# Kernel optimization log

Measured on AMD Instinct MI355X. Metric: run time of the kernel, lower is better.

Reference implementation:

```python
import jax, jax.numpy as jnp
import numpy as np

B, T, H = 1, 2048, 1024
NH, HD, NKV = 16, 64, 4
G = NH // NKV                    # kv groups == Mamba2 n_groups
SINK, WIN = 128, 256             # attention sinks, sliding window
STATE, KSIZE = 256, 4            # Mamba2 state size, conv kernel
MINT = H                         # Mamba2 intermediate (expand=1) == NH*HD
CONV_DIM = MINT + 2 * G * STATE  # 3072
D_INPROJ = MINT + CONV_DIM + NH  # 4112
INTER = 4096
EPS = 1e-6


def _rmsnorm(x, w):
    v = jnp.mean(jnp.square(x), axis=-1, keepdims=True)
    return x * jax.lax.rsqrt(v + EPS) * w


def _rot_half(t):
    return jnp.concatenate([-t[..., HD // 2:], t[..., :HD // 2]], axis=-1)


def _mamba2(h, in_proj_w, conv_w, conv_b, dt_bias, A_log, Dp, mnorm_w, mout_w):
    # h: [B, L, H] evicted hidden states
    Bm, Lm, _ = h.shape
    proj = h @ in_proj_w                                   # [B,L,D_INPROJ]
    z, xBC, dt = jnp.split(proj, [MINT, MINT + CONV_DIM], axis=-1)
    # causal depthwise conv1d (kernel KSIZE), then SiLU
    xp = jnp.pad(xBC, ((0, 0), (KSIZE - 1, 0), (0, 0)))
    conv = sum(xp[:, k:k + Lm, :] * conv_w[:, k] for k in range(KSIZE)) + conv_b
    xBC = jax.nn.silu(conv)
    xs, Bc, Cc = jnp.split(xBC, [MINT, MINT + G * STATE], axis=-1)
    xs = xs.reshape(Bm, Lm, NH, HD)
    Bc = jnp.repeat(Bc.reshape(Bm, Lm, G, STATE), NH // G, axis=2)  # group->head
    Cc = jnp.repeat(Cc.reshape(Bm, Lm, G, STATE), NH // G, axis=2)
    dt = jax.nn.softplus(dt + dt_bias)                     # [B,L,NH]
    A = -jnp.exp(A_log)                                    # [NH]

    def step(hst, inp):
        xt, bt, ct, dtt = inp  # [B,NH,HD],[B,NH,N],[B,NH,N],[B,NH]
        dA = jnp.exp(dtt * A)[..., None, None]
        hst = hst * dA + (dtt[..., None] * xt)[..., None] * bt[:, :, None, :]
        yt = jnp.einsum('bhdn,bhn->bhd', hst, ct)
        return hst, yt

    h0 = jnp.zeros((Bm, NH, HD, STATE), h.dtype)
    tm = lambda a: jnp.moveaxis(a, 1, 0)
    _, ys = jax.lax.scan(step, h0, (tm(xs), tm(Bc), tm(Cc), tm(dt)))
    y = jnp.moveaxis(ys, 0, 1) + Dp[None, None, :, None] * xs
    y = y.reshape(Bm, Lm, MINT) * jax.nn.silu(z)           # gated
    y = _rmsnorm(y, mnorm_w)
    return y @ mout_w


def _forward(hidden_states, cos, sin, ln1_w, q_w, q_b, k_w, k_b, v_w, v_b, o_w,
             in_proj_w, conv_w, conv_b, dt_bias, A_log, D, mnorm_w, mout_w,
             ln2_w, gate_w, up_w, down_w):
    x = hidden_states
    hn = _rmsnorm(x, ln1_w)
    evict_end = T - WIN
    evicted = hn[:, SINK:evict_end]                       # [B, overflow, H]
    mem_out = _mamba2(evicted, in_proj_w, conv_w, conv_b, dt_bias, A_log, D,
                      mnorm_w, mout_w)                    # [B, overflow, H]
    mem_act = mem_out[:, -1:, :]                          # compressed-memory token
    hc = jnp.concatenate([hn[:, :SINK], mem_act, hn[:, evict_end:]], axis=1)
    cosc = jnp.concatenate([cos[:, :SINK + 1], cos[:, evict_end:]], axis=1)
    sinc = jnp.concatenate([sin[:, :SINK + 1], sin[:, evict_end:]], axis=1)
    Tc = SINK + 1 + WIN                                   # 385 compacted tokens
    q = (hc @ q_w + q_b).reshape(B, Tc, NH, HD)
    k = (hc @ k_w + k_b).reshape(B, Tc, NKV, HD)
    v = (hc @ v_w + v_b).reshape(B, Tc, NKV, HD)
    q = q * cosc[:, :, None, :] + _rot_half(q) * sinc[:, :, None, :]
    k = k * cosc[:, :, None, :] + _rot_half(k) * sinc[:, :, None, :]
    k = jnp.repeat(k, G, axis=2)                          # GQA expand
    v = jnp.repeat(v, G, axis=2)
    scores = jnp.einsum('bqhd,bkhd->bhqk', q, k) * (HD ** -0.5)
    idx = jnp.arange(Tc)
    causal = idx[:, None] >= idx[None, :]
    scores = jnp.where(causal, scores, jnp.finfo(scores.dtype).min)
    attn = jax.nn.softmax(scores, axis=-1)
    ao = jnp.einsum('bhqk,bkhd->bqhd', attn, v).reshape(B, Tc, H)
    # replace mem token output with the full Mamba2 outputs for evicted tokens
    ao = jnp.concatenate([ao[:, :SINK], mem_out, ao[:, SINK + 1:]], axis=1)
    ao = ao @ o_w                                         # [B, T, H]
    h1 = x + ao
    mlp_in = _rmsnorm(h1, ln2_w)
    mlp = (jax.nn.silu(mlp_in @ gate_w) * (mlp_in @ up_w)) @ down_w
    return h1 + mlp


def setup_inputs() -> dict:
    key = jax.random.key(0)
    ks = list(jax.random.split(key, 16))
    def nrm(i, shape, s=0.02):
        return jax.random.normal(ks[i], shape, jnp.float32) * s
    x = jax.random.normal(ks[0], (B, T, H), jnp.float32)
    pos = jnp.arange(T, dtype=jnp.float32)
    inv = 1.0 / (10000.0 ** (jnp.arange(0, HD, 2, dtype=jnp.float32) / HD))
    ang = pos[:, None] * inv[None, :]
    emb = jnp.concatenate([ang, ang], axis=-1)
    cos = jnp.broadcast_to(jnp.cos(emb)[None], (B, T, HD))
    sin = jnp.broadcast_to(jnp.sin(emb)[None], (B, T, HD))
    return {
        'hidden_states': x, 'cos': cos, 'sin': sin,
        'ln1_w': jnp.ones((H,), jnp.float32),
        'q_w': nrm(1, (H, NH * HD)), 'q_b': jnp.zeros((NH * HD,), jnp.float32),
        'k_w': nrm(2, (H, NKV * HD)), 'k_b': jnp.zeros((NKV * HD,), jnp.float32),
        'v_w': nrm(3, (H, NKV * HD)), 'v_b': jnp.zeros((NKV * HD,), jnp.float32),
        'o_w': nrm(4, (NH * HD, H)),
        'in_proj_w': nrm(5, (H, D_INPROJ)),
        'conv_w': nrm(6, (CONV_DIM, KSIZE), 0.2),
        'conv_b': jnp.zeros((CONV_DIM,), jnp.float32),
        'dt_bias': nrm(7, (NH,), 0.5),
        'A_log': jnp.log(jnp.arange(1, NH + 1, dtype=jnp.float32)),
        'D': jnp.ones((NH,), jnp.float32),
        'mnorm_w': jnp.ones((MINT,), jnp.float32),
        'mout_w': nrm(8, (MINT, H)),
        'ln2_w': jnp.ones((H,), jnp.float32),
        'gate_w': nrm(9, (H, INTER)),
        'up_w': nrm(10, (H, INTER)),
        'down_w': nrm(11, (INTER, H)),
    }


def reference(hidden_states, cos, sin, ln1_w, q_w, q_b, k_w, k_b, v_w, v_b, o_w,
              in_proj_w, conv_w, conv_b, dt_bias, A_log, D, mnorm_w, mout_w,
              ln2_w, gate_w, up_w, down_w):
    return _forward(hidden_states, cos, sin, ln1_w, q_w, q_b, k_w, k_b, v_w,
                    v_b, o_w, in_proj_w, conv_w, conv_b, dt_bias, A_log, D,
                    mnorm_w, mout_w, ln2_w, gate_w, up_w, down_w)
```

## Files before the change

kernel.cpp:

```cpp
#include <hip/hip_runtime.h>
#include <hip/hip_bf16.h>
#include <math.h>

#define TLEN 2048
#define HDIM 1024
#define NHEAD 16
#define HEADD 64
#define NKVH 4
#define SINKN 128
#define WINN 256
#define STATEN 256
#define KCONV 4
#define MINTN 1024
#define CONVD 3072
#define DPROJ 4112
#define INTERN 4096
#define LMN 1664
#define TCN 385
#define EPSF 1e-6f
#define SCHUNK 128
#define NCHUNK 13

__device__ __forceinline__ float siluf(float x){ return x / (1.0f + expf(-x)); }
__device__ __forceinline__ float softplusf_(float x){ return fmaxf(x, 0.0f) + log1pf(expf(-fabsf(x))); }

__device__ __forceinline__ float block_sum256(float v, float* sb){
#pragma unroll
  for (int m = 32; m > 0; m >>= 1) v += __shfl_xor(v, m);
  int wid = threadIdx.x >> 6;
  if ((threadIdx.x & 63) == 0) sb[wid] = v;
  __syncthreads();
  return sb[0] + sb[1] + sb[2] + sb[3];
}

__global__ __launch_bounds__(256) void rmsnorm_k(const float* __restrict__ in, const float* __restrict__ w,
                                                 float* __restrict__ out){
  __shared__ float sb[4];
  size_t r = blockIdx.x;
  float4 x = ((const float4*)(in + r*HDIM))[threadIdx.x];
  float ss = block_sum256(x.x*x.x + x.y*x.y + x.z*x.z + x.w*x.w, sb);
  float sc = 1.0f / sqrtf(ss*(1.0f/HDIM) + EPSF);
  float4 wv = ((const float4*)w)[threadIdx.x];
  ((float4*)(out + r*HDIM))[threadIdx.x] =
      make_float4(x.x*sc*wv.x, x.y*sc*wv.y, x.z*sc*wv.z, x.w*sc*wv.w);
}

__global__ __launch_bounds__(256) void gated_rmsnorm_k(const float* __restrict__ ys, const float* __restrict__ proj,
                                                       const float* __restrict__ w, float* __restrict__ out){
  __shared__ float sb[4];
  size_t r = blockIdx.x;
  float4 y = ((const float4*)(ys + r*MINTN))[threadIdx.x];
  float4 z = ((const float4*)(proj + r*DPROJ))[threadIdx.x];
  y.x *= siluf(z.x); y.y *= siluf(z.y); y.z *= siluf(z.z); y.w *= siluf(z.w);
  float ss = block_sum256(y.x*y.x + y.y*y.y + y.z*y.z + y.w*y.w, sb);
  float sc = 1.0f / sqrtf(ss*(1.0f/MINTN) + EPSF);
  float4 wv = ((const float4*)w)[threadIdx.x];
  ((float4*)(out + r*MINTN))[threadIdx.x] =
      make_float4(y.x*sc*wv.x, y.y*sc*wv.y, y.z*sc*wv.z, y.w*sc*wv.w);
}

template<int EPI>
__global__ __launch_bounds__(256) void gemm_k(const float* __restrict__ A, const float* __restrict__ B,
                                              float* __restrict__ C, const float* __restrict__ bias,
                                              const float* __restrict__ extra, int M, int N, int K){
  __shared__ float As[16][132];
  __shared__ float Bs[16][64];
  int tid = threadIdx.x;
  int tx = tid & 15, ty = tid >> 4;
  int m0 = blockIdx.y * 128, n0 = blockIdx.x * 64;
  int ar = tid >> 2, ak = (tid & 3) * 4;
  int bk = tid >> 4, bn = (tid & 15) * 4;
  float acc[8][4];
#pragma unroll
  for (int i = 0; i < 8; i++)
#pragma unroll
    for (int j = 0; j < 4; j++) acc[i][j] = 0.f;

  for (int k0 = 0; k0 < K; k0 += 16){
    float4 a0 = make_float4(0,0,0,0), a1 = make_float4(0,0,0,0), b0 = make_float4(0,0,0,0);
    if (m0 + ar < M)      a0 = *(const float4*)(A + (size_t)(m0+ar)*K + k0 + ak);
    if (m0 + ar + 64 < M) a1 = *(const float4*)(A + (size_t)(m0+ar+64)*K + k0 + ak);
    if (n0 + bn < N)      b0 = *(const float4*)(B + (size_t)(k0+bk)*N + n0 + bn);
    __syncthreads();
    As[ak+0][ar] = a0.x; As[ak+1][ar] = a0.y; As[ak+2][ar] = a0.z; As[ak+3][ar] = a0.w;
    As[ak+0][ar+64] = a1.x; As[ak+1][ar+64] = a1.y; As[ak+2][ar+64] = a1.z; As[ak+3][ar+64] = a1.w;
    *(float4*)&Bs[bk][bn] = b0;
    __syncthreads();
#pragma unroll
    for (int kk = 0; kk < 16; kk++){
      float a[8], b[4];
      *(float4*)(a)   = *(const float4*)&As[kk][ty*8];
      *(float4*)(a+4) = *(const float4*)&As[kk][ty*8+4];
      *(float4*)(b)   = *(const float4*)&Bs[kk][tx*4];
#pragma unroll
      for (int i = 0; i < 8; i++)
#pragma unroll
        for (int j = 0; j < 4; j++) acc[i][j] = fmaf(a[i], b[j], acc[i][j]);
    }
  }
  int n = n0 + tx*4;
  if (n >= N) return;
#pragma unroll
  for (int i = 0; i < 8; i++){
    int m = m0 + ty*8 + i;
    if (m >= M) break;
    float r0 = acc[i][0], r1 = acc[i][1], r2 = acc[i][2], r3 = acc[i][3];
    if (EPI == 1){ r0 += bias[n]; r1 += bias[n+1]; r2 += bias[n+2]; r3 += bias[n+3]; }
    if (EPI == 2){ const float* e = extra + (size_t)m*N + n; r0 += e[0]; r1 += e[1]; r2 += e[2]; r3 += e[3]; }
    *(float4*)(C + (size_t)m*N + n) = make_float4(r0, r1, r2, r3);
  }
}

template<int EPI>
__global__ __launch_bounds__(256) void gemm64_k(const float* __restrict__ A, const float* __restrict__ B,
                                                float* __restrict__ C, const float* __restrict__ bias,
                                                const float* __restrict__ extra, int M, int N, int K){
  __shared__ float As[16][68];
  __shared__ float Bs[16][64];
  int tid = threadIdx.x;
  int tx = tid & 15, ty = tid >> 4;
  int m0 = blockIdx.y * 64, n0 = blockIdx.x * 64;
  int ar = tid >> 2, ak = (tid & 3) * 4;
  int bk = tid >> 4, bn = (tid & 15) * 4;
  float acc[4][4];
#pragma unroll
  for (int i = 0; i < 4; i++)
#pragma unroll
    for (int j = 0; j < 4; j++) acc[i][j] = 0.f;

  for (int k0 = 0; k0 < K; k0 += 16){
    float4 a0 = make_float4(0,0,0,0);
    if (m0 + ar < M) a0 = *(const float4*)(A + (size_t)(m0+ar)*K + k0 + ak);
    float4 b0 = *(const float4*)(B + (size_t)(k0+bk)*N + n0 + bn);
    __syncthreads();
    As[ak+0][ar] = a0.x; As[ak+1][ar] = a0.y; As[ak+2][ar] = a0.z; As[ak+3][ar] = a0.w;
    *(float4*)&Bs[bk][bn] = b0;
    __syncthreads();
#pragma unroll
    for (int kk = 0; kk < 16; kk++){
      float a[4], b[4];
      *(float4*)(a) = *(const float4*)&As[kk][ty*4];
      *(float4*)(b) = *(const float4*)&Bs[kk][tx*4];
#pragma unroll
      for (int i = 0; i < 4; i++)
#pragma unroll
        for (int j = 0; j < 4; j++) acc[i][j] = fmaf(a[i], b[j], acc[i][j]);
    }
  }
  int n = n0 + tx*4;
#pragma unroll
  for (int i = 0; i < 4; i++){
    int m = m0 + ty*4 + i;
    if (m >= M) break;
    float r0 = acc[i][0], r1 = acc[i][1], r2 = acc[i][2], r3 = acc[i][3];
    if (EPI == 1){ r0 += bias[n]; r1 += bias[n+1]; r2 += bias[n+2]; r3 += bias[n+3]; }
    if (EPI == 2){ const float* e = extra + (size_t)m*N + n; r0 += e[0]; r1 += e[1]; r2 += e[2]; r3 += e[3]; }
    *(float4*)(C + (size_t)m*N + n) = make_float4(r0, r1, r2, r3);
  }
}

__global__ __launch_bounds__(256) void gemm_gateup_k(const float* __restrict__ A, const float* __restrict__ G,
                                                     const float* __restrict__ U, float* __restrict__ C,
                                                     int M, int N, int K){
  __shared__ float As[16][132];
  __shared__ float Gs[16][64];
  __shared__ float Us[16][64];
  int tid = threadIdx.x;
  int tx = tid & 15, ty = tid >> 4;
  int m0 = blockIdx.y * 128, n0 = blockIdx.x * 64;
  int ar = tid >> 2, ak = (tid & 3) * 4;
  int bk = tid >> 4, bn = (tid & 15) * 4;
  float accg[8][4], accu[8][4];
#pragma unroll
  for (int i = 0; i < 8; i++)
#pragma unroll
    for (int j = 0; j < 4; j++){ accg[i][j] = 0.f; accu[i][j] = 0.f; }

  for (int k0 = 0; k0 < K; k0 += 16){
    float4 a0 = *(const float4*)(A + (size_t)(m0+ar)*K + k0 + ak);
    float4 a1 = *(const float4*)(A + (size_t)(m0+ar+64)*K + k0 + ak);
    float4 g0 = *(const float4*)(G + (size_t)(k0+bk)*N + n0 + bn);
    float4 u0 = *(const float4*)(U + (size_t)(k0+bk)*N + n0 + bn);
    __syncthreads();
    As[ak+0][ar] = a0.x; As[ak+1][ar] = a0.y; As[ak+2][ar] = a0.z; As[ak+3][ar] = a0.w;
    As[ak+0][ar+64] = a1.x; As[ak+1][ar+64] = a1.y; As[ak+2][ar+64] = a1.z; As[ak+3][ar+64] = a1.w;
    *(float4*)&Gs[bk][bn] = g0;
    *(float4*)&Us[bk][bn] = u0;
    __syncthreads();
#pragma unroll
    for (int kk = 0; kk < 16; kk++){
      float a[8], g[4], u[4];
      *(float4*)(a)   = *(const float4*)&As[kk][ty*8];
      *(float4*)(a+4) = *(const float4*)&As[kk][ty*8+4];
      *(float4*)(g)   = *(const float4*)&Gs[kk][tx*4];
      *(float4*)(u)   = *(const float4*)&Us[kk][tx*4];
#pragma unroll
      for (int i = 0; i < 8; i++)
#pragma unroll
        for (int j = 0; j < 4; j++){
          accg[i][j] = fmaf(a[i], g[j], accg[i][j]);
          accu[i][j] = fmaf(a[i], u[j], accu[i][j]);
        }
    }
  }
  int n = n0 + tx*4;
#pragma unroll
  for (int i = 0; i < 8; i++){
    int m = m0 + ty*8 + i;
    *(float4*)(C + (size_t)m*N + n) =
        make_float4(siluf(accg[i][0])*accu[i][0], siluf(accg[i][1])*accu[i][1],
                    siluf(accg[i][2])*accu[i][2], siluf(accg[i][3])*accu[i][3]);
  }
}

__global__ __launch_bounds__(256) void conv_silu_k(const float* __restrict__ proj, const float* __restrict__ cw,
                                                   const float* __restrict__ cb, float* __restrict__ out){
  int idx = blockIdx.x*256 + threadIdx.x;
  if (idx >= LMN*CONVD) return;
  int c = idx % CONVD;
  int t = idx / CONVD;
  float acc = cb[c];
#pragma unroll
  for (int kk = 0; kk < KCONV; kk++){
    int ts = t + kk - (KCONV-1);
    if (ts >= 0) acc = fmaf(proj[(size_t)ts*DPROJ + MINTN + c], cw[c*KCONV + kk], acc);
  }
  out[idx] = siluf(acc);
}

__global__ __launch_bounds__(256) void dtprep_k(const float* __restrict__ proj, const float* __restrict__ dtb,
                                                const float* __restrict__ alog, float* __restrict__ dt,
                                                float* __restrict__ dA){
  int idx = blockIdx.x*256 + threadIdx.x;
  if (idx >= LMN*NHEAD) return;
  int h = idx & 15, t = idx >> 4;
  float d = softplusf_(proj[(size_t)t*DPROJ + MINTN + CONVD + h] + dtb[h]);
  dt[idx] = d;
  dA[idx] = expf(-d * expf(alog[h]));
}


__global__ __launch_bounds__(64) void chunk_prod_k(const float* __restrict__ dAb, float* __restrict__ aQ){
  int c = blockIdx.x >> 4, h = blockIdx.x & 15;
  int lane = threadIdx.x;
  float p = dAb[(c*SCHUNK + lane)*NHEAD + h] * dAb[(c*SCHUNK + 64 + lane)*NHEAD + h];
#pragma unroll
  for (int m = 32; m > 0; m >>= 1) p *= __shfl_xor(p, m);
  if (lane == 0) aQ[c*NHEAD + h] = p;
}

__global__ __launch_bounds__(256) void scan_local_k(const float* __restrict__ cv, const float* __restrict__ dtb,
                                                    const float* __restrict__ dAb, float* __restrict__ hloc){
  int c = blockIdx.x >> 6;
  int sub = blockIdx.x & 63;
  int h = sub >> 2;
  int d = (sub & 3)*16 + (threadIdx.x >> 4);
  int nc = threadIdx.x & 15;
  int g = h >> 2;
  const float* xp = cv + h*HEADD + d;
  const float* Bp = cv + MINTN + g*STATEN + nc*16;
  int t0 = c*SCHUNK;
  float s[16];
#pragma unroll
  for (int i = 0; i < 16; i++) s[i] = 0.f;

  float4 B0[4], B1[4];
  float x0, dt0, dA0, x1, dt1, dA1;
  {
    size_t o = (size_t)t0*CONVD;
    x0 = xp[o]; dt0 = dtb[t0*NHEAD + h]; dA0 = dAb[t0*NHEAD + h];
    B0[0]=((const float4*)(Bp+o))[0]; B0[1]=((const float4*)(Bp+o))[1];
    B0[2]=((const float4*)(Bp+o))[2]; B0[3]=((const float4*)(Bp+o))[3];
    o = (size_t)(t0+1)*CONVD;
    x1 = xp[o]; dt1 = dtb[(t0+1)*NHEAD + h]; dA1 = dAb[(t0+1)*NHEAD + h];
    B1[0]=((const float4*)(Bp+o))[0]; B1[1]=((const float4*)(Bp+o))[1];
    B1[2]=((const float4*)(Bp+o))[2]; B1[3]=((const float4*)(Bp+o))[3];
  }
  for (int tt = 0; tt < SCHUNK; tt += 2){
    {
      float coef = dt0 * x0;
      const float* bf = (const float*)B0;
#pragma unroll
      for (int i = 0; i < 16; i++) s[i] = fmaf(s[i], dA0, coef*bf[i]);
      int tn = t0 + ((tt+2 < SCHUNK) ? tt+2 : SCHUNK-1);
      size_t o = (size_t)tn*CONVD;
      x0 = xp[o]; dt0 = dtb[tn*NHEAD + h]; dA0 = dAb[tn*NHEAD + h];
      B0[0]=((const float4*)(Bp+o))[0]; B0[1]=((const float4*)(Bp+o))[1];
      B0[2]=((const float4*)(Bp+o))[2]; B0[3]=((const float4*)(Bp+o))[3];
    }
    {
      float coef = dt1 * x1;
      const float* bf = (const float*)B1;
#pragma unroll
      for (int i = 0; i < 16; i++) s[i] = fmaf(s[i], dA1, coef*bf[i]);
      int tn = t0 + ((tt+3 < SCHUNK) ? tt+3 : SCHUNK-1);
      size_t o = (size_t)tn*CONVD;
      x1 = xp[o]; dt1 = dtb[tn*NHEAD + h]; dA1 = dAb[tn*NHEAD + h];
      B1[0]=((const float4*)(Bp+o))[0]; B1[1]=((const float4*)(Bp+o))[1];
      B1[2]=((const float4*)(Bp+o))[2]; B1[3]=((const float4*)(Bp+o))[3];
    }
  }
  size_t base = ((size_t)(c*NHEAD + h)*STATEN + nc*16)*64 + d;
#pragma unroll
  for (int i = 0; i < 16; i++) hloc[base + (size_t)i*64] = s[i];
}

__global__ __launch_bounds__(256) void chunk_combine_k(float* __restrict__ hloc, const float* __restrict__ aQ){
  int e = blockIdx.x*256 + threadIdx.x;
  int h = e >> 14;
  float s = 0.f;
  for (int c = 0; c < NCHUNK; c++){
    float a = aQ[c*NHEAD + h];
    size_t off = (size_t)c*(NHEAD*STATEN*64) + e;
    float tmp = hloc[off];
    hloc[off] = s;
    s = fmaf(s, a, tmp);
  }
}

__global__ __launch_bounds__(256) void scan_out_k(const float* __restrict__ cv, const float* __restrict__ dtb,
                                                  const float* __restrict__ dAb, const float* __restrict__ Dp,
                                                  const float* __restrict__ hstart, float* __restrict__ ys){
  int c = blockIdx.x >> 6;
  int sub = blockIdx.x & 63;
  int h = sub >> 2;
  int d = (sub & 3)*16 + (threadIdx.x >> 4);
  int nc = threadIdx.x & 15;
  int g = h >> 2;
  const float* xp = cv + h*HEADD + d;
  const float* Bp = cv + MINTN + g*STATEN + nc*16;
  const float* Cp = cv + MINTN + 1024 + g*STATEN + nc*16;
  float Dh = Dp[h];
  int t0 = c*SCHUNK;
  float s[16];
  {
    size_t base = ((size_t)(c*NHEAD + h)*STATEN + nc*16)*64 + d;
#pragma unroll
    for (int i = 0; i < 16; i++) s[i] = hstart[base + (size_t)i*64];
  }

  float4 B0[4], C0[4], B1[4], C1[4];
  float x0, dt0, dA0, x1, dt1, dA1;
  {
    size_t o = (size_t)t0*CONVD;
    x0 = xp[o]; dt0 = dtb[t0*NHEAD + h]; dA0 = dAb[t0*NHEAD + h];
    B0[0]=((const float4*)(Bp+o))[0]; B0[1]=((const float4*)(Bp+o))[1];
    B0[2]=((const float4*)(Bp+o))[2]; B0[3]=((const float4*)(Bp+o))[3];
    C0[0]=((const float4*)(Cp+o))[0]; C0[1]=((const float4*)(Cp+o))[1];
    C0[2]=((const float4*)(Cp+o))[2]; C0[3]=((const float4*)(Cp+o))[3];
    o = (size_t)(t0+1)*CONVD;
    x1 = xp[o]; dt1 = dtb[(t0+1)*NHEAD + h]; dA1 = dAb[(t0+1)*NHEAD + h];
    B1[0]=((const float4*)(Bp+o))[0]; B1[1]=((const float4*)(Bp+o))[1];
    B1[2]=((const float4*)(Bp+o))[2]; B1[3]=((const float4*)(Bp+o))[3];
    C1[0]=((const float4*)(Cp+o))[0]; C1[1]=((const float4*)(Cp+o))[1];
    C1[2]=((const float4*)(Cp+o))[2]; C1[3]=((const float4*)(Cp+o))[3];
  }
  for (int tt = 0; tt < SCHUNK; tt += 2){
    {
      int t = t0 + tt;
      float coef = dt0 * x0;
      float accp[4] = {0.f,0.f,0.f,0.f};
      const float* bf = (const float*)B0;
      const float* cf = (const float*)C0;
#pragma unroll
      for (int i = 0; i < 16; i++){
        s[i] = fmaf(s[i], dA0, coef*bf[i]);
        accp[i & 3] = fmaf(s[i], cf[i], accp[i & 3]);
      }
      float accv = (accp[0]+accp[1])+(accp[2]+accp[3]);
      accv += __shfl_xor(accv, 1); accv += __shfl_xor(accv, 2);
      accv += __shfl_xor(accv, 4); accv += __shfl_xor(accv, 8);
      if (nc == 0) ys[(size_t)t*MINTN + h*HEADD + d] = accv + Dh*x0;
      int tn = t0 + ((tt+2 < SCHUNK) ? tt+2 : SCHUNK-1);
      size_t o = (size_t)tn*CONVD;
      x0 = xp[o]; dt0 = dtb[tn*NHEAD + h]; dA0 = dAb[tn*NHEAD + h];
      B0[0]=((const float4*)(Bp+o))[0]; B0[1]=((const float4*)(Bp+o))[1];
      B0[2]=((const float4*)(Bp+o))[2]; B0[3]=((const float4*)(Bp+o))[3];
      C0[0]=((const float4*)(Cp+o))[0]; C0[1]=((const float4*)(Cp+o))[1];
      C0[2]=((const float4*)(Cp+o))[2]; C0[3]=((const float4*)(Cp+o))[3];
    }
    {
      int t = t0 + tt + 1;
      float coef = dt1 * x1;
      float accp[4] = {0.f,0.f,0.f,0.f};
      const float* bf = (const float*)B1;
      const float* cf = (const float*)C1;
#pragma unroll
      for (int i = 0; i < 16; i++){
        s[i] = fmaf(s[i], dA1, coef*bf[i]);
        accp[i & 3] = fmaf(s[i], cf[i], accp[i & 3]);
      }
      float accv = (accp[0]+accp[1])+(accp[2]+accp[3]);
      accv += __shfl_xor(accv, 1); accv += __shfl_xor(accv, 2);
      accv += __shfl_xor(accv, 4); accv += __shfl_xor(accv, 8);
      if (nc == 0) ys[(size_t)t*MINTN + h*HEADD + d] = accv + Dh*x1;
      int tn = t0 + ((tt+3 < SCHUNK) ? tt+3 : SCHUNK-1);
      size_t o = (size_t)tn*CONVD;
      x1 = xp[o]; dt1 = dtb[tn*NHEAD + h]; dA1 = dAb[tn*NHEAD + h];
      B1[0]=((const float4*)(Bp+o))[0]; B1[1]=((const float4*)(Bp+o))[1];
      B1[2]=((const float4*)(Bp+o))[2]; B1[3]=((const float4*)(Bp+o))[3];
      C1[0]=((const float4*)(Cp+o))[0]; C1[1]=((const float4*)(Cp+o))[1];
      C1[2]=((const float4*)(Cp+o))[2]; C1[3]=((const float4*)(Cp+o))[3];
    }
  }
}

__global__ __launch_bounds__(256) void build_hc_k(const float* __restrict__ hn, const float* __restrict__ memo,
                                                  float* __restrict__ hc){
  int idx = blockIdx.x*256 + threadIdx.x;
  if (idx >= TCN*HDIM) return;
  int r = idx >> 10, c = idx & 1023;
  float v;
  if (r < SINKN)        v = hn[(size_t)r*HDIM + c];
  else if (r == SINKN)  v = memo[(size_t)(LMN-1)*HDIM + c];
  else                  v = hn[(size_t)(r + 1663)*HDIM + c];
  hc[idx] = v;
}

__global__ __launch_bounds__(256) void rope_k(float* __restrict__ q, float* __restrict__ k,
                                              const float* __restrict__ cosp, const float* __restrict__ sinp){
  int idx = blockIdx.x*256 + threadIdx.x;
  if (idx >= TCN*20*32) return;
  int dd = idx & 31;
  int hh = (idx >> 5) % 20;
  int t  = idx / (20*32);
  int ci = (t <= SINKN) ? t : t + 1663;
  float* p = (hh < NHEAD) ? (q + (size_t)t*HDIM + hh*HEADD)
                          : (k + (size_t)t*(NKVH*HEADD) + (hh - NHEAD)*HEADD);
  float a = p[dd], b = p[dd+32];
  float c0 = cosp[(size_t)ci*HEADD + dd], c1 = cosp[(size_t)ci*HEADD + dd + 32];
  float s0 = sinp[(size_t)ci*HEADD + dd], s1 = sinp[(size_t)ci*HEADD + dd + 32];
  p[dd]    = a*c0 - b*s0;
  p[dd+32] = b*c1 + a*s1;
}

__global__ __launch_bounds__(256) void attn_k(const float* __restrict__ q, const float* __restrict__ k,
                                              const float* __restrict__ v, float* __restrict__ aoc){
  __shared__ float Qs[64][65];
  __shared__ float Ks[64][65];
  __shared__ float Vs[64][68];
  int qt = blockIdx.x, h = blockIdx.y;
  int tid = threadIdx.x;
  int ql = tid >> 2, dg = tid & 3;
  int qg = qt*64 + ql;
  int kvh = h >> 2;
#pragma unroll
  for (int i = 0; i < 16; i++){
    int idx = tid + 256*i;
    int r = idx >> 6, c = idx & 63;
    int qr = qt*64 + r;
    Qs[r][c] = (qr < TCN) ? q[(size_t)qr*HDIM + h*HEADD + c] : 0.f;
  }
  __syncthreads();
  float qreg[64];
#pragma unroll
  for (int d2 = 0; d2 < 64; d2++) qreg[d2] = Qs[ql][d2];
  __syncthreads();

  float mrun = -INFINITY, lrun = 0.f;
  float acc[16];
#pragma unroll
  for (int i = 0; i < 16; i++) acc[i] = 0.f;

  for (int kt = 0; kt <= qt; kt++){
    __syncthreads();
#pragma unroll
    for (int i = 0; i < 16; i++){
      int idx = tid + 256*i;
      int r = idx >> 6, c = idx & 63;
      int kr = kt*64 + r;
      float kv = 0.f, vv = 0.f;
      if (kr < TCN){
        kv = k[(size_t)kr*(NKVH*HEADD) + kvh*HEADD + c];
        vv = v[(size_t)kr*(NKVH*HEADD) + kvh*HEADD + c];
      }
      Ks[r][c] = kv; Vs[r][c] = vv;
    }
    __syncthreads();
    float p[16]; float tmax = -INFINITY;
#pragma unroll
    for (int jj = 0; jj < 16; jj++){
      int j = jj*4 + dg;
      float sv = 0.f;
#pragma unroll
      for (int d2 = 0; d2 < 64; d2++) sv = fmaf(qreg[d2], Ks[j][d2], sv);
      sv *= 0.125f;
      int kr = kt*64 + j;
      if (kr > qg || kr >= TCN) sv = -INFINITY;
      p[jj] = sv;
      tmax = fmaxf(tmax, sv);
    }
    tmax = fmaxf(tmax, __shfl_xor(tmax, 1));
    tmax = fmaxf(tmax, __shfl_xor(tmax, 2));
    float nm = fmaxf(mrun, tmax);
    if (nm == -INFINITY) nm = 0.f;
    float sc = expf(mrun - nm);
    float sump = 0.f;
#pragma unroll
    for (int jj = 0; jj < 16; jj++){ p[jj] = expf(p[jj] - nm); sump += p[jj]; }
    sump += __shfl_xor(sump, 1);
    sump += __shfl_xor(sump, 2);
    lrun = lrun*sc + sump;
    mrun = nm;
#pragma unroll
    for (int i = 0; i < 16; i++) acc[i] *= sc;
#pragma unroll
    for (int jj = 0; jj < 16; jj++) Qs[ql][jj*4 + dg] = p[jj];
    __syncthreads();
#pragma unroll
    for (int j = 0; j < 64; j++){
      float pv = Qs[ql][j];
#pragma unroll
      for (int c4 = 0; c4 < 4; c4++){
        float4 vv = *(const float4*)&Vs[j][dg*16 + c4*4];
        acc[c4*4+0] = fmaf(pv, vv.x, acc[c4*4+0]);
        acc[c4*4+1] = fmaf(pv, vv.y, acc[c4*4+1]);
        acc[c4*4+2] = fmaf(pv, vv.z, acc[c4*4+2]);
        acc[c4*4+3] = fmaf(pv, vv.w, acc[c4*4+3]);
      }
    }
  }
  if (qg < TCN){
    float inv = 1.0f / lrun;
#pragma unroll
    for (int c4 = 0; c4 < 4; c4++){
      *(float4*)(aoc + (size_t)qg*HDIM + h*HEADD + dg*16 + c4*4) =
          make_float4(acc[c4*4]*inv, acc[c4*4+1]*inv, acc[c4*4+2]*inv, acc[c4*4+3]*inv);
    }
  }
}

__global__ __launch_bounds__(256) void build_ao_k(const float* __restrict__ aoc, const float* __restrict__ memo,
                                                  float* __restrict__ aof){
  int idx = blockIdx.x*256 + threadIdx.x;
  if (idx >= TLEN*HDIM) return;
  int r = idx >> 10, c = idx & 1023;
  float v;
  if (r < SINKN)              v = aoc[(size_t)r*HDIM + c];
  else if (r < TLEN - WINN)   v = memo[(size_t)(r - SINKN)*HDIM + c];
  else                        v = aoc[(size_t)(r - 1663)*HDIM + c];
  aof[idx] = v;
}

extern "C" void kernel_launch(void* const* d_in, const int* in_sizes, int n_in,
                              void* d_out, int out_size, void* d_ws, size_t ws_size,
                              hipStream_t stream){
  (void)in_sizes; (void)n_in; (void)out_size; (void)ws_size;
  const float* x      = (const float*)d_in[0];
  const float* cosp   = (const float*)d_in[1];
  const float* sinp   = (const float*)d_in[2];
  const float* ln1_w  = (const float*)d_in[3];
  const float* q_w    = (const float*)d_in[4];
  const float* q_b    = (const float*)d_in[5];
  const float* k_w    = (const float*)d_in[6];
  const float* k_b    = (const float*)d_in[7];
  const float* v_w    = (const float*)d_in[8];
  const float* v_b    = (const float*)d_in[9];
  const float* o_w    = (const float*)d_in[10];
  const float* inpw   = (const float*)d_in[11];
  const float* convw  = (const float*)d_in[12];
  const float* convb  = (const float*)d_in[13];
  const float* dtbias = (const float*)d_in[14];
  const float* alog   = (const float*)d_in[15];
  const float* Dp     = (const float*)d_in[16];
  const float* mnw    = (const float*)d_in[17];
  const float* moutw  = (const float*)d_in[18];
  const float* ln2_w  = (const float*)d_in[19];
  const float* gatew  = (const float*)d_in[20];
  const float* upw    = (const float*)d_in[21];
  const float* downw  = (const float*)d_in[22];
  float* out = (float*)d_out;

  float* w     = (float*)d_ws;
  float* hn    = w + 0;
  float* proj  = w + 2097152;
  float* conv  = w + 8939520;
  float* memo  = w + 8939520;
  float* mamx  = w + 10643456;
  float* dtb   = w + 14051328;
  float* dAb   = w + 14077952;
  float* yscan = w + 14104576;
  float* hc    = w + 14104576;
  float* qb    = w + 14498816;
  float* kb    = w + 14893056;
  float* vb    = w + 14991616;
  float* aoc   = w + 15090176;
  float* hloc  = w + 15808512;
  float* aQ    = w + 19216384;
  float* aof   = w + 2097152;
  float* h1    = w + 0;
  float* mlpin = w + 2097152;
  float* gu    = w + 4194304;

  rmsnorm_k<<<TLEN, 256, 0, stream>>>(x, ln1_w, hn);
  gemm_k<0><<<dim3(65, 13), 256, 0, stream>>>(hn + (size_t)SINKN*HDIM, inpw, proj, nullptr, nullptr, LMN, DPROJ, HDIM);
  conv_silu_k<<<(LMN*CONVD + 255)/256, 256, 0, stream>>>(proj, convw, convb, conv);
  dtprep_k<<<(LMN*NHEAD + 255)/256, 256, 0, stream>>>(proj, dtbias, alog, dtb, dAb);
  chunk_prod_k<<<NCHUNK*NHEAD, 64, 0, stream>>>(dAb, aQ);
  scan_local_k<<<NCHUNK*64, 256, 0, stream>>>(conv, dtb, dAb, hloc);
  chunk_combine_k<<<1024, 256, 0, stream>>>(hloc, aQ);
  scan_out_k<<<NCHUNK*64, 256, 0, stream>>>(conv, dtb, dAb, Dp, hloc, yscan);
  gated_rmsnorm_k<<<LMN, 256, 0, stream>>>(yscan, proj, mnw, mamx);
  gemm64_k<0><<<dim3(16, 26), 256, 0, stream>>>(mamx, moutw, memo, nullptr, nullptr, LMN, HDIM, HDIM);
  build_hc_k<<<(TCN*HDIM + 255)/256, 256, 0, stream>>>(hn, memo, hc);
  gemm64_k<1><<<dim3(16, 7), 256, 0, stream>>>(hc, q_w, qb, q_b, nullptr, TCN, HDIM, HDIM);
  gemm64_k<1><<<dim3(4, 7), 256, 0, stream>>>(hc, k_w, kb, k_b, nullptr, TCN, NKVH*HEADD, HDIM);
  gemm64_k<1><<<dim3(4, 7), 256, 0, stream>>>(hc, v_w, vb, v_b, nullptr, TCN, NKVH*HEADD, HDIM);
  rope_k<<<(TCN*20*32 + 255)/256, 256, 0, stream>>>(qb, kb, cosp, sinp);
  attn_k<<<dim3(7, 16), 256, 0, stream>>>(qb, kb, vb, aoc);
  build_ao_k<<<(TLEN*HDIM + 255)/256, 256, 0, stream>>>(aoc, memo, aof);
  gemm64_k<2><<<dim3(16, 32), 256, 0, stream>>>(aof, o_w, h1, nullptr, x, TLEN, HDIM, HDIM);
  rmsnorm_k<<<TLEN, 256, 0, stream>>>(h1, ln2_w, mlpin);
  gemm_gateup_k<<<dim3(64, 16), 256, 0, stream>>>(mlpin, gatew, upw, gu, TLEN, INTERN, HDIM);
  gemm64_k<2><<<dim3(16, 32), 256, 0, stream>>>(gu, downw, out, nullptr, h1, TLEN, HDIM, INTERN);
}
```

Before: 2.006 ms.

## Switch large fp32 GEMMs to split-bf16 MFMA with three-product emulation

```diff
diff --git a/kernel.cpp b/kernel.cpp
--- a/kernel.cpp
+++ b/kernel.cpp
@@ -21,8 +21,13 @@
 #define SCHUNK 128
 #define NCHUNK 13
 
+typedef __attribute__((ext_vector_type(8))) short bf16x8;
+typedef __attribute__((ext_vector_type(4))) float f32x4;
+
 __device__ __forceinline__ float siluf(float x){ return x / (1.0f + expf(-x)); }
 __device__ __forceinline__ float softplusf_(float x){ return fmaxf(x, 0.0f) + log1pf(expf(-fabsf(x))); }
+__device__ __forceinline__ unsigned short bftr(float x){ return (unsigned short)(__float_as_uint(x) >> 16); }
+__device__ __forceinline__ float bfval(unsigned short h){ return __uint_as_float(((unsigned int)h) << 16); }
 
 __device__ __forceinline__ float block_sum256(float v, float* sb){
 #pragma unroll
@@ -60,55 +65,105 @@
 }
 
 template<int EPI>
-__global__ __launch_bounds__(256) void gemm_k(const float* __restrict__ A, const float* __restrict__ B,
-                                              float* __restrict__ C, const float* __restrict__ bias,
-                                              const float* __restrict__ extra, int M, int N, int K){
-  __shared__ float As[16][132];
-  __shared__ float Bs[16][64];
+__global__ __launch_bounds__(256) void mfma_gemm_k(const float* __restrict__ A, const float* __restrict__ B,
+                                                   float* C, const float* extra,
+                                                   int M, int N, int K){
+  __shared__ unsigned short Ah[128*40], Al[128*40], Bh[128*40], Bl[128*40];
   int tid = threadIdx.x;
-  int tx = tid & 15, ty = tid >> 4;
-  int m0 = blockIdx.y * 128, n0 = blockIdx.x * 64;
-  int ar = tid >> 2, ak = (tid & 3) * 4;
-  int bk = tid >> 4, bn = (tid & 15) * 4;
-  float acc[8][4];
-#pragma unroll
-  for (int i = 0; i < 8; i++)
-#pragma unroll
-    for (int j = 0; j < 4; j++) acc[i][j] = 0.f;
-
-  for (int k0 = 0; k0 < K; k0 += 16){
-    float4 a0 = make_float4(0,0,0,0), a1 = make_float4(0,0,0,0), b0 = make_float4(0,0,0,0);
-    if (m0 + ar < M)      a0 = *(const float4*)(A + (size_t)(m0+ar)*K + k0 + ak);
-    if (m0 + ar + 64 < M) a1 = *(const float4*)(A + (size_t)(m0+ar+64)*K + k0 + ak);
-    if (n0 + bn < N)      b0 = *(const float4*)(B + (size_t)(k0+bk)*N + n0 + bn);
+  int lane = tid & 63, wid = tid >> 6;
+  int wr = (wid >> 1) * 64, wc = (wid & 1) * 64;
+  int lr = lane & 15, kg = lane >> 4;
+  int m0 = blockIdx.y * 128, n0 = blockIdx.x * 128;
+
+  int arow = tid >> 1, akc = (tid & 1) * 16;
+  int bp = tid >> 4;
+  int ba = tid & 15;
+
+  f32x4 acc[4][4];
+#pragma unroll
+  for (int i = 0; i < 4; i++)
+#pragma unroll
+    for (int j = 0; j < 4; j++) acc[i][j] = (f32x4){0.f, 0.f, 0.f, 0.f};
+
+  for (int k0 = 0; k0 < K; k0 += 32){
+    const float* ap = A + (size_t)(m0 + arow)*K + k0 + akc;
+    float4 av0 = *(const float4*)(ap);
+    float4 av1 = *(const float4*)(ap + 4);
+    float4 av2 = *(const float4*)(ap + 8);
+    float4 av3 = *(const float4*)(ap + 12);
+    const float* b0p = B + (size_t)(k0 + 2*bp)*N + n0;
+    const float* b1p = b0p + N;
+    float xb0[8], xb1[8];
+#pragma unroll
+    for (int j = 0; j < 8; j++){
+      int b = (j + ba) & 7;
+      int col = ba*8 + b;
+      bool ok = (n0 + col) < N;
+      xb0[j] = ok ? b0p[col] : 0.f;
+      xb1[j] = ok ? b1p[col] : 0.f;
+    }
     __syncthreads();
-    As[ak+0][ar] = a0.x; As[ak+1][ar] = a0.y; As[ak+2][ar] = a0.z; As[ak+3][ar] = a0.w;
-    As[ak+0][ar+64] = a1.x; As[ak+1][ar+64] = a1.y; As[ak+2][ar+64] = a1.z; As[ak+3][ar+64] = a1.w;
-    *(float4*)&Bs[bk][bn] = b0;
+    {
+      float va[16] = {av0.x,av0.y,av0.z,av0.w, av1.x,av1.y,av1.z,av1.w,
+                      av2.x,av2.y,av2.z,av2.w, av3.x,av3.y,av3.z,av3.w};
+      bf16x8 vh0, vh1, vl0, vl1;
+#pragma unroll
+      for (int e = 0; e < 8; e++){
+        unsigned short h0 = bftr(va[e]);     vh0[e] = (short)h0;
+        vl0[e] = (short)bftr(va[e] - bfval(h0));
+        unsigned short h1 = bftr(va[e+8]);   vh1[e] = (short)h1;
+        vl1[e] = (short)bftr(va[e+8] - bfval(h1));
+      }
+      int ai = arow*40 + akc;
+      *(bf16x8*)&Ah[ai] = vh0; *(bf16x8*)&Ah[ai+8] = vh1;
+      *(bf16x8*)&Al[ai] = vl0; *(bf16x8*)&Al[ai+8] = vl1;
+    }
+#pragma unroll
+    for (int j = 0; j < 8; j++){
+      int b = (j + ba) & 7;
+      int col = ba*8 + b;
+      unsigned short h0 = bftr(xb0[j]), h1 = bftr(xb1[j]);
+      unsigned int hh = (unsigned int)h0 | ((unsigned int)h1 << 16);
+      unsigned short l0 = bftr(xb0[j] - bfval(h0)), l1 = bftr(xb1[j] - bfval(h1));
+      unsigned int ll = (unsigned int)l0 | ((unsigned int)l1 << 16);
+      *(unsigned int*)&Bh[col*40 + 2*bp] = hh;
+      *(unsigned int*)&Bl[col*40 + 2*bp] = ll;
+    }
     __syncthreads();
-#pragma unroll
-    for (int kk = 0; kk < 16; kk++){
-      float a[8], b[4];
-      *(float4*)(a)   = *(const float4*)&As[kk][ty*8];
-      *(float4*)(a+4) = *(const float4*)&As[kk][ty*8+4];
-      *(float4*)(b)   = *(const float4*)&Bs[kk][tx*4];
-#pragma unroll
-      for (int i = 0; i < 8; i++)
-#pragma unroll
-        for (int j = 0; j < 4; j++) acc[i][j] = fmaf(a[i], b[j], acc[i][j]);
-    }
-  }
-  int n = n0 + tx*4;
-  if (n >= N) return;
-#pragma unroll
-  for (int i = 0; i < 8; i++){
-    int m = m0 + ty*8 + i;
-    if (m >= M) break;
-    float r0 = acc[i][0], r1 = acc[i][1], r2 = acc[i][2], r3 = acc[i][3];
-    if (EPI == 1){ r0 += bias[n]; r1 += bias[n+1]; r2 += bias[n+2]; r3 += bias[n+3]; }
-    if (EPI == 2){ const float* e = extra + (size_t)m*N + n; r0 += e[0]; r1 += e[1]; r2 += e[2]; r3 += e[3]; }
-    *(float4*)(C + (size_t)m*N + n) = make_float4(r0, r1, r2, r3);
-  }
+    bf16x8 fah[4], fal[4], fbh[4], fbl[4];
+#pragma unroll
+    for (int f = 0; f < 4; f++){
+      int ai = (wr + f*16 + lr)*40 + kg*8;
+      fah[f] = *(const bf16x8*)&Ah[ai];
+      fal[f] = *(const bf16x8*)&Al[ai];
+      int bi = (wc + f*16 + lr)*40 + kg*8;
+      fbh[f] = *(const bf16x8*)&Bh[bi];
+      fbl[f] = *(const bf16x8*)&Bl[bi];
+    }
+#pragma unroll
+    for (int fr = 0; fr < 4; fr++)
+#pragma unroll
+      for (int fc = 0; fc < 4; fc++){
+        acc[fr][fc] = __builtin_amdgcn_mfma_f32_16x16x32_bf16(fal[fr], fbh[fc], acc[fr][fc], 0, 0, 0);
+        acc[fr][fc] = __builtin_amdgcn_mfma_f32_16x16x32_bf16(fah[fr], fbl[fc], acc[fr][fc], 0, 0, 0);
+        acc[fr][fc] = __builtin_amdgcn_mfma_f32_16x16x32_bf16(fah[fr], fbh[fc], acc[fr][fc], 0, 0, 0);
+      }
+  }
+#pragma unroll
+  for (int fr = 0; fr < 4; fr++)
+#pragma unroll
+    for (int fc = 0; fc < 4; fc++)
+#pragma unroll
+      for (int j = 0; j < 4; j++){
+        int row = m0 + wr + fr*16 + kg*4 + j;
+        int col = n0 + wc + fc*16 + lr;
+        if (col < N){
+          float r = acc[fr][fc][j];
+          if (EPI == 2) r += extra[(size_t)row*N + col];
+          if (EPI == 3) r *= siluf(extra[(size_t)row*N + col]);
+          C[(size_t)row*N + col] = r;
+        }
+      }
 }
 
 template<int EPI>
@@ -159,60 +214,6 @@
   }
 }
 
-__global__ __launch_bounds__(256) void gemm_gateup_k(const float* __restrict__ A, const float* __restrict__ G,
-                                                     const float* __restrict__ U, float* __restrict__ C,
-                                                     int M, int N, int K){
-  __shared__ float As[16][132];
-  __shared__ float Gs[16][64];
-  __shared__ float Us[16][64];
-  int tid = threadIdx.x;
-  int tx = tid & 15, ty = tid >> 4;
-  int m0 = blockIdx.y * 128, n0 = blockIdx.x * 64;
-  int ar = tid >> 2, ak = (tid & 3) * 4;
-  int bk = tid >> 4, bn = (tid & 15) * 4;
-  float accg[8][4], accu[8][4];
-#pragma unroll
-  for (int i = 0; i < 8; i++)
-#pragma unroll
-    for (int j = 0; j < 4; j++){ accg[i][j] = 0.f; accu[i][j] = 0.f; }
-
-  for (int k0 = 0; k0 < K; k0 += 16){
-    float4 a0 = *(const float4*)(A + (size_t)(m0+ar)*K + k0 + ak);
-    float4 a1 = *(const float4*)(A + (size_t)(m0+ar+64)*K + k0 + ak);
-    float4 g0 = *(const float4*)(G + (size_t)(k0+bk)*N + n0 + bn);
-    float4 u0 = *(const float4*)(U + (size_t)(k0+bk)*N + n0 + bn);
-    __syncthreads();
-    As[ak+0][ar] = a0.x; As[ak+1][ar] = a0.y; As[ak+2][ar] = a0.z; As[ak+3][ar] = a0.w;
-    As[ak+0][ar+64] = a1.x; As[ak+1][ar+64] = a1.y; As[ak+2][ar+64] = a1.z; As[ak+3][ar+64] = a1.w;
-    *(float4*)&Gs[bk][bn] = g0;
-    *(float4*)&Us[bk][bn] = u0;
-    __syncthreads();
-#pragma unroll
-    for (int kk = 0; kk < 16; kk++){
-      float a[8], g[4], u[4];
-      *(float4*)(a)   = *(const float4*)&As[kk][ty*8];
-      *(float4*)(a+4) = *(const float4*)&As[kk][ty*8+4];
-      *(float4*)(g)   = *(const float4*)&Gs[kk][tx*4];
-      *(float4*)(u)   = *(const float4*)&Us[kk][tx*4];
-#pragma unroll
-      for (int i = 0; i < 8; i++)
-#pragma unroll
-        for (int j = 0; j < 4; j++){
-          accg[i][j] = fmaf(a[i], g[j], accg[i][j]);
-          accu[i][j] = fmaf(a[i], u[j], accu[i][j]);
-        }
-    }
-  }
-  int n = n0 + tx*4;
-#pragma unroll
-  for (int i = 0; i < 8; i++){
-    int m = m0 + ty*8 + i;
-    *(float4*)(C + (size_t)m*N + n) =
-        make_float4(siluf(accg[i][0])*accu[i][0], siluf(accg[i][1])*accu[i][1],
-                    siluf(accg[i][2])*accu[i][2], siluf(accg[i][3])*accu[i][3]);
-  }
-}
-
 __global__ __launch_bounds__(256) void conv_silu_k(const float* __restrict__ proj, const float* __restrict__ cw,
                                                    const float* __restrict__ cb, float* __restrict__ out){
   int idx = blockIdx.x*256 + threadIdx.x;
@@ -238,7 +239,6 @@
   dt[idx] = d;
   dA[idx] = expf(-d * expf(alog[h]));
 }
-
 
 __global__ __launch_bounds__(64) void chunk_prod_k(const float* __restrict__ dAb, float* __restrict__ aQ){
   int c = blockIdx.x >> 4, h = blockIdx.x & 15;
@@ -590,10 +590,10 @@
   float* aof   = w + 2097152;
   float* h1    = w + 0;
   float* mlpin = w + 2097152;
-  float* gu    = w + 4194304;
+  float* gbuf  = w + 4194304;
 
   rmsnorm_k<<<TLEN, 256, 0, stream>>>(x, ln1_w, hn);
-  gemm_k<0><<<dim3(65, 13), 256, 0, stream>>>(hn + (size_t)SINKN*HDIM, inpw, proj, nullptr, nullptr, LMN, DPROJ, HDIM);
+  mfma_gemm_k<0><<<dim3(33, 13), 256, 0, stream>>>(hn + (size_t)SINKN*HDIM, inpw, proj, nullptr, LMN, DPROJ, HDIM);
   conv_silu_k<<<(LMN*CONVD + 255)/256, 256, 0, stream>>>(proj, convw, convb, conv);
   dtprep_k<<<(LMN*NHEAD + 255)/256, 256, 0, stream>>>(proj, dtbias, alog, dtb, dAb);
   chunk_prod_k<<<NCHUNK*NHEAD, 64, 0, stream>>>(dAb, aQ);
@@ -601,7 +601,7 @@
   chunk_combine_k<<<1024, 256, 0, stream>>>(hloc, aQ);
   scan_out_k<<<NCHUNK*64, 256, 0, stream>>>(conv, dtb, dAb, Dp, hloc, yscan);
   gated_rmsnorm_k<<<LMN, 256, 0, stream>>>(yscan, proj, mnw, mamx);
-  gemm64_k<0><<<dim3(16, 26), 256, 0, stream>>>(mamx, moutw, memo, nullptr, nullptr, LMN, HDIM, HDIM);
+  mfma_gemm_k<0><<<dim3(8, 13), 256, 0, stream>>>(mamx, moutw, memo, nullptr, LMN, HDIM, HDIM);
   build_hc_k<<<(TCN*HDIM + 255)/256, 256, 0, stream>>>(hn, memo, hc);
   gemm64_k<1><<<dim3(16, 7), 256, 0, stream>>>(hc, q_w, qb, q_b, nullptr, TCN, HDIM, HDIM);
   gemm64_k<1><<<dim3(4, 7), 256, 0, stream>>>(hc, k_w, kb, k_b, nullptr, TCN, NKVH*HEADD, HDIM);
@@ -609,8 +609,9 @@
   rope_k<<<(TCN*20*32 + 255)/256, 256, 0, stream>>>(qb, kb, cosp, sinp);
   attn_k<<<dim3(7, 16), 256, 0, stream>>>(qb, kb, vb, aoc);
   build_ao_k<<<(TLEN*HDIM + 255)/256, 256, 0, stream>>>(aoc, memo, aof);
-  gemm64_k<2><<<dim3(16, 32), 256, 0, stream>>>(aof, o_w, h1, nullptr, x, TLEN, HDIM, HDIM);
+  mfma_gemm_k<2><<<dim3(8, 16), 256, 0, stream>>>(aof, o_w, h1, x, TLEN, HDIM, HDIM);
   rmsnorm_k<<<TLEN, 256, 0, stream>>>(h1, ln2_w, mlpin);
-  gemm_gateup_k<<<dim3(64, 16), 256, 0, stream>>>(mlpin, gatew, upw, gu, TLEN, INTERN, HDIM);
-  gemm64_k<2><<<dim3(16, 32), 256, 0, stream>>>(gu, downw, out, nullptr, h1, TLEN, HDIM, INTERN);
-}
+  mfma_gemm_k<0><<<dim3(32, 16), 256, 0, stream>>>(mlpin, gatew, gbuf, nullptr, TLEN, INTERN, HDIM);
+  mfma_gemm_k<3><<<dim3(32, 16), 256, 0, stream>>>(mlpin, upw, gbuf, gbuf, TLEN, INTERN, HDIM);
+  mfma_gemm_k<2><<<dim3(8, 16), 256, 0, stream>>>(gbuf, downw, out, h1, TLEN, HDIM, INTERN);
+}
```

Measured after the change: 1.752 ms. 1.14x faster.
